# Performance work log

Measured on AMD Instinct MI355X. Metric: run time of the kernel, lower is better.

## Reference

```python
import jax, jax.numpy as jnp
import numpy as np

N, D = 8192, 128
ALPHA = 2.0


def setup_inputs() -> dict:
    key = jax.random.key(0)
    k1, k2, k3, k4 = jax.random.split(key, 4)
    z_au = jax.random.normal(k1, (N, D), dtype=jnp.float32)
    z_tp = jax.random.normal(k2, (N, D), dtype=jnp.float32)
    fc_weights = jax.random.normal(k3, (2, D), dtype=jnp.float32)
    labels = jax.random.randint(k4, (N,), 0, 2, dtype=jnp.int64)
    return {"z_au": z_au, "z_tp": z_tp, "fc_weights": fc_weights, "labels": labels}


def reference(z_au, z_tp, fc_weights, labels):
    # labels is unused in the (intended) math; kept for signature fidelity.
    n = z_au.shape[0]
    neg_inf = jnp.finfo(z_au.dtype).min
    eye = jnp.eye(n, dtype=bool)

    # pairwise dot-product similarities (cosim == raw matmul in the source)
    s_aa = z_au @ z_au.T              # [n, n]
    s_tt = z_tp @ z_tp.T              # [n, n]
    s_at = z_au @ z_tp.T              # [n, n]

    # pos_loss(i) = log( sum_{j!=i} exp(au_i.au_j) + exp(tp_i.tp_j) )
    pos_logits = jnp.concatenate(
        [jnp.where(eye, neg_inf, s_aa), jnp.where(eye, neg_inf, s_tt)], axis=1
    )                                  # [n, 2n]
    pos = jax.nn.logsumexp(pos_logits, axis=1)          # [n]

    # neg_loss(i) = log( sum_{j!=i} exp(au_i.tp_j) )
    neg = jax.nn.logsumexp(jnp.where(eye, neg_inf, s_at), axis=1)  # [n]

    # alpha * cosim(au_i, tp_i)
    au_tp_diag = jnp.einsum("nd,nd->n", z_au, z_tp)      # [n]

    supcon = jnp.sum(-pos + neg + ALPHA * au_tp_diag)

    # prototype loss: reward same-class prototype, punish other-class prototype
    pt0, pt1 = fc_weights[0], fc_weights[1]
    pt_loss = jnp.sum(-z_au @ pt0 + z_au @ pt1 - z_tp @ pt1 + z_tp @ pt0) / n

    return (pt_loss + supcon) / (n + 2)
```

## Files before the change

kernel.cpp:

```cpp
#include <hip/hip_runtime.h>


typedef float f32x4 __attribute__((ext_vector_type(4)));
typedef __bf16 bf16x8 __attribute__((ext_vector_type(8)));

static constexpr int   N_ROWS = 8192;
static constexpr int   DIM    = 128;
static constexpr float SQRT_LOG2E = 1.2011224087864498f;
static constexpr float C2  = 32.0f;
static constexpr float LN2 = 0.6931471805599453f;


__device__ inline unsigned short f2bf_rne(float x) {
    unsigned u = __builtin_bit_cast(unsigned, x);
    u += 0x7fffu + ((u >> 16) & 1u);
    return (unsigned short)(u >> 16);
}

#define GLD16(gptr, lptr)                                                  \
    __builtin_amdgcn_global_load_lds(                                      \
        (const __attribute__((address_space(1))) void*)(gptr),             \
        (__attribute__((address_space(3))) void*)(lptr), 16, 0, 0)

__global__ void prep_kernel(const float* __restrict__ zau,
                            const float* __restrict__ ztp,
                            unsigned short* __restrict__ bau,
                            unsigned short* __restrict__ btp,
                            float* __restrict__ P, float* __restrict__ Ng,
                            float* __restrict__ acc, unsigned* __restrict__ done) {
    int gid  = blockIdx.x * blockDim.x + threadIdx.x;
    int base = gid * 4;
    float4 a = *reinterpret_cast<const float4*>(zau + base);
    float4 t = *reinterpret_cast<const float4*>(ztp + base);
    ushort4 ua, ut;
    ua.x = f2bf_rne(a.x * SQRT_LOG2E); ua.y = f2bf_rne(a.y * SQRT_LOG2E);
    ua.z = f2bf_rne(a.z * SQRT_LOG2E); ua.w = f2bf_rne(a.w * SQRT_LOG2E);
    ut.x = f2bf_rne(t.x * SQRT_LOG2E); ut.y = f2bf_rne(t.y * SQRT_LOG2E);
    ut.z = f2bf_rne(t.z * SQRT_LOG2E); ut.w = f2bf_rne(t.w * SQRT_LOG2E);
    *reinterpret_cast<ushort4*>(bau + base) = ua;
    *reinterpret_cast<ushort4*>(btp + base) = ut;
    if (gid < N_ROWS) { P[gid] = 0.0f; Ng[gid] = 0.0f; }
    if (gid == 0)     { acc[0] = 0.0f; acc[1] = 0.0f; done[0] = 0u; }
}

template<bool DIAG>
__device__ inline void accum2(const f32x4 (&a)[2][2], float (&dst)[2][4],
                              int r0w, int colp, int quad, int l15) {
#pragma unroll
    for (int mt = 0; mt < 2; mt++)
#pragma unroll
        for (int nt = 0; nt < 2; nt++)
#pragma unroll
            for (int r = 0; r < 4; r++) {
                float e = __builtin_amdgcn_exp2f(a[mt][nt][r]);
                if (DIAG) {
                    int grow = r0w + mt * 16 + quad * 4 + r;
                    int gcol = colp + nt * 16 + l15;
                    if (grow == gcol) e = 0.0f;
                }
                dst[mt][r] += e;
            }
}

__global__ __launch_bounds__(256, 3)
void score_kernel(const unsigned short* __restrict__ bau,
                  const unsigned short* __restrict__ btp,
                  float* __restrict__ P, float* __restrict__ Ng) {
    __shared__ __align__(16) unsigned short ldsA[16 * 512];
    __shared__ __align__(16) unsigned short ldsT[16 * 512];

    const int tid  = threadIdx.x;
    const int lane = tid & 63;
    const int wave = tid >> 6;
    const int quad = lane >> 4;
    const int l15  = lane & 15;
    const int rb   = blockIdx.x & 63;
    const int cs   = blockIdx.x >> 6;
    const int r0w  = rb * 128 + wave * 32;

    const int laneoff = l15 * 256 + quad * 16;


    bf16x8 aAu[2][4], aTp[2][4];
#pragma unroll
    for (int mt = 0; mt < 2; mt++) {
        int row = r0w + mt * 16 + l15;
        const unsigned short* pa = bau + row * DIM + quad * 8;
        const unsigned short* pt = btp + row * DIM + quad * 8;
#pragma unroll
        for (int k = 0; k < 4; k++) {
            aAu[mt][k] = *reinterpret_cast<const bf16x8*>(pa + k * 32);
            aTp[mt][k] = *reinterpret_cast<const bf16x8*>(pt + k * 32);
        }
    }

    float sP[2][4] = {{0.f,0.f,0.f,0.f},{0.f,0.f,0.f,0.f}};
    float sN[2][4] = {{0.f,0.f,0.f,0.f},{0.f,0.f,0.f,0.f}};

    for (int ct = 0; ct < 8; ct++) {
        const int colbase = cs * 512 + ct * 64;
        __syncthreads();
#pragma unroll
        for (int j = 0; j < 8; j++) {
            const int f   = wave * 8 + j;
            const int arr = f >> 4;
            const int nt  = (f >> 2) & 3;
            const int k   = f & 3;
            const char* gb = (const char*)(arr ? btp : bau)
                           + ((size_t)(colbase + nt * 16) << 8) + (k << 6);
            unsigned short* lb = (arr ? ldsT : ldsA) + ((nt * 4 + k) << 9);
            GLD16(gb + laneoff, lb);
        }
        __syncthreads();

        const bool diag = (colbase < r0w + 32) && (colbase + 64 > r0w);

#pragma unroll
        for (int np = 0; np < 2; np++) {
            f32x4 acc[2][2];
#pragma unroll
            for (int mt = 0; mt < 2; mt++)
#pragma unroll
                for (int nt = 0; nt < 2; nt++)
                    acc[mt][nt] = f32x4{-C2, -C2, -C2, -C2};
#pragma unroll
            for (int k = 0; k < 4; k++) {
                bf16x8 b0 = *reinterpret_cast<const bf16x8*>(
                    ldsA + (((np * 2 + 0) * 4 + k) << 9) + lane * 8);
                bf16x8 b1 = *reinterpret_cast<const bf16x8*>(
                    ldsA + (((np * 2 + 1) * 4 + k) << 9) + lane * 8);
#pragma unroll
                for (int mt = 0; mt < 2; mt++) {
                    acc[mt][0] = __builtin_amdgcn_mfma_f32_16x16x32_bf16(
                        aAu[mt][k], b0, acc[mt][0], 0, 0, 0);
                    acc[mt][1] = __builtin_amdgcn_mfma_f32_16x16x32_bf16(
                        aAu[mt][k], b1, acc[mt][1], 0, 0, 0);
                }
            }
            if (diag) accum2<true >(acc, sP, r0w, colbase + np * 32, quad, l15);
            else      accum2<false>(acc, sP, r0w, colbase + np * 32, quad, l15);
        }

#pragma unroll
        for (int np = 0; np < 2; np++) {
            f32x4 aT[2][2], aX[2][2];
#pragma unroll
            for (int mt = 0; mt < 2; mt++)
#pragma unroll
                for (int nt = 0; nt < 2; nt++) {
                    aT[mt][nt] = f32x4{-C2, -C2, -C2, -C2};
                    aX[mt][nt] = f32x4{-C2, -C2, -C2, -C2};
                }
#pragma unroll
            for (int k = 0; k < 4; k++) {
                bf16x8 b0 = *reinterpret_cast<const bf16x8*>(
                    ldsT + (((np * 2 + 0) * 4 + k) << 9) + lane * 8);
                bf16x8 b1 = *reinterpret_cast<const bf16x8*>(
                    ldsT + (((np * 2 + 1) * 4 + k) << 9) + lane * 8);
#pragma unroll
                for (int mt = 0; mt < 2; mt++) {
                    aT[mt][0] = __builtin_amdgcn_mfma_f32_16x16x32_bf16(
                        aTp[mt][k], b0, aT[mt][0], 0, 0, 0);
                    aX[mt][0] = __builtin_amdgcn_mfma_f32_16x16x32_bf16(
                        aAu[mt][k], b0, aX[mt][0], 0, 0, 0);
                    aT[mt][1] = __builtin_amdgcn_mfma_f32_16x16x32_bf16(
                        aTp[mt][k], b1, aT[mt][1], 0, 0, 0);
                    aX[mt][1] = __builtin_amdgcn_mfma_f32_16x16x32_bf16(
                        aAu[mt][k], b1, aX[mt][1], 0, 0, 0);
                }
            }
            if (diag) { accum2<true >(aT, sP, r0w, colbase + np * 32, quad, l15);
                        accum2<true >(aX, sN, r0w, colbase + np * 32, quad, l15); }
            else      { accum2<false>(aT, sP, r0w, colbase + np * 32, quad, l15);
                        accum2<false>(aX, sN, r0w, colbase + np * 32, quad, l15); }
        }
    }

#pragma unroll
    for (int mt = 0; mt < 2; mt++)
#pragma unroll
        for (int r = 0; r < 4; r++) {
            float p = sP[mt][r], ng = sN[mt][r];
            for (int m = 1; m < 16; m <<= 1) {
                p  += __shfl_xor(p,  m, 64);
                ng += __shfl_xor(ng, m, 64);
            }
            if (l15 == 0) {
                int row = r0w + mt * 16 + quad * 4 + r;
                atomicAdd(&P[row],  p);
                atomicAdd(&Ng[row], ng);
            }
        }
}

__global__ void finalize_kernel(const float* __restrict__ zau,
                                const float* __restrict__ ztp,
                                const float* __restrict__ fc,
                                const float* __restrict__ P,
                                const float* __restrict__ Ng,
                                float* __restrict__ acc,
                                unsigned* __restrict__ done,
                                float* __restrict__ out) {
    int tid     = threadIdx.x;
    int lane    = tid & 63;
    int wave_id = blockIdx.x * 4 + (tid >> 6);

    float2 w0 = *reinterpret_cast<const float2*>(fc + 2 * lane);
    float2 w1 = *reinterpret_cast<const float2*>(fc + 256 + 2 * lane);
    float wx = w1.x - w0.x, wy = w1.y - w0.y;

    float ptp = 0.0f, ssum = 0.0f;
    for (int j = 0; j < 8; j++) {
        int i = wave_id * 8 + j;
        float2 a = *reinterpret_cast<const float2*>(zau + i * DIM + 2 * lane);
        float2 t = *reinterpret_cast<const float2*>(ztp + i * DIM + 2 * lane);
        float d = a.x * t.x + a.y * t.y;
        ptp += (a.x - t.x) * wx + (a.y - t.y) * wy;
        for (int m = 1; m < 64; m <<= 1) d += __shfl_xor(d, m, 64);
        if (lane == 0) {
            float c = LN2 * (__builtin_amdgcn_logf(Ng[i]) -
                             __builtin_amdgcn_logf(P[i])) + 2.0f * d;
            ssum += c;
        }
    }
    for (int m = 1; m < 64; m <<= 1) ptp += __shfl_xor(ptp, m, 64);
    if (lane == 0) {
        atomicAdd(&acc[0], ssum);
        atomicAdd(&acc[1], ptp);
    }

    __syncthreads();
    if (tid == 0) {
        __threadfence();
        unsigned ticket = atomicAdd(done, 1u);
        if (ticket == gridDim.x - 1) {
            float a0 = atomicAdd(&acc[0], 0.0f);
            float a1 = atomicAdd(&acc[1], 0.0f);
            out[0] = (a1 / (float)N_ROWS + a0) / (float)(N_ROWS + 2);
        }
    }
}

extern "C" void kernel_launch(void* const* d_in, const int* in_sizes, int n_in,
                              void* d_out, int out_size, void* d_ws, size_t ws_size,
                              hipStream_t stream) {
    const float* zau = (const float*)d_in[0];
    const float* ztp = (const float*)d_in[1];
    const float* fc  = (const float*)d_in[2];
    float* out = (float*)d_out;

    char* ws = (char*)d_ws;
    unsigned short* bau = (unsigned short*)(ws);
    unsigned short* btp = (unsigned short*)(ws + 2097152);
    float*    P    = (float*)(ws + 4194304);
    float*    Ng   = (float*)(ws + 4227072);
    float*    acc  = (float*)(ws + 4259840);
    unsigned* done = (unsigned*)(ws + 4259848);

    prep_kernel<<<dim3(1024), dim3(256), 0, stream>>>(zau, ztp, bau, btp, P, Ng, acc, done);
    score_kernel<<<dim3(1024), dim3(256), 0, stream>>>(bau, btp, P, Ng);
    finalize_kernel<<<dim3(256), dim3(256), 0, stream>>>(zau, ztp, fc, P, Ng, acc, done, out);
}
```

Measured before the change: 158.4 us.

## Software-pipeline exp accumulation of previous tile behind next tile's loads

Halves the column tile from 64 to 32 and merges the two LDS buffers into one. Each tile's three score blocks (AA, TT, AT) are now kept in registers and exponentiated on the next iteration, while the next tile's global-to-LDS loads are in flight. The aim is to hide load latency and barrier stalls behind the exp2 work and to free LDS for higher occupancy. The cost is twice as many barrier rounds and more live accumulator registers. The first iteration also exponentiates the initial -C2 placeholder blocks, which adds a small spurious term to each row's sums.

```diff
diff --git a/kernel.cpp b/kernel.cpp
--- a/kernel.cpp
+++ b/kernel.cpp
@@ -44,7 +44,7 @@
 }
 
 template<bool DIAG>
-__device__ inline void accum2(const f32x4 (&a)[2][2], float (&dst)[2][4],
+__device__ inline void expacc(const f32x4 (&a)[2][2], float (&dst)[2][4],
                               int r0w, int colp, int quad, int l15) {
 #pragma unroll
     for (int mt = 0; mt < 2; mt++)
@@ -66,8 +66,7 @@
 void score_kernel(const unsigned short* __restrict__ bau,
                   const unsigned short* __restrict__ btp,
                   float* __restrict__ P, float* __restrict__ Ng) {
-    __shared__ __align__(16) unsigned short ldsA[16 * 512];
-    __shared__ __align__(16) unsigned short ldsT[16 * 512];
+    __shared__ __align__(16) unsigned short lds[16 * 512];
 
     const int tid  = threadIdx.x;
     const int lane = tid & 63;
@@ -80,7 +79,6 @@
 
     const int laneoff = l15 * 256 + quad * 16;
 
-
     bf16x8 aAu[2][4], aTp[2][4];
 #pragma unroll
     for (int mt = 0; mt < 2; mt++) {
@@ -97,82 +95,96 @@
     float sP[2][4] = {{0.f,0.f,0.f,0.f},{0.f,0.f,0.f,0.f}};
     float sN[2][4] = {{0.f,0.f,0.f,0.f},{0.f,0.f,0.f,0.f}};
 
-    for (int ct = 0; ct < 8; ct++) {
-        const int colbase = cs * 512 + ct * 64;
+    f32x4 pAA[2][2], pTT[2][2], pAT[2][2];
+#pragma unroll
+    for (int mt = 0; mt < 2; mt++)
+#pragma unroll
+        for (int nt = 0; nt < 2; nt++) {
+            pAA[mt][nt] = f32x4{-C2, -C2, -C2, -C2};
+            pTT[mt][nt] = f32x4{-C2, -C2, -C2, -C2};
+            pAT[mt][nt] = f32x4{-C2, -C2, -C2, -C2};
+        }
+    int prevcol = -100000;
+
+    for (int ct = 0; ct < 16; ct++) {
+        const int colbase = cs * 512 + ct * 32;
+
         __syncthreads();
 #pragma unroll
-        for (int j = 0; j < 8; j++) {
-            const int f   = wave * 8 + j;
-            const int arr = f >> 4;
-            const int nt  = (f >> 2) & 3;
+        for (int j = 0; j < 4; j++) {
+            const int f   = wave * 4 + j;
+            const int arr = f >> 3;
+            const int nt  = (f >> 2) & 1;
             const int k   = f & 3;
             const char* gb = (const char*)(arr ? btp : bau)
                            + ((size_t)(colbase + nt * 16) << 8) + (k << 6);
-            unsigned short* lb = (arr ? ldsT : ldsA) + ((nt * 4 + k) << 9);
-            GLD16(gb + laneoff, lb);
-        }
+            GLD16(gb + laneoff, lds + (f << 9));
+        }
+
+        {
+            const bool pd = (prevcol < r0w + 32) && (prevcol + 32 > r0w);
+            if (pd) {
+                expacc<true >(pAA, sP, r0w, prevcol, quad, l15);
+                expacc<true >(pTT, sP, r0w, prevcol, quad, l15);
+                expacc<true >(pAT, sN, r0w, prevcol, quad, l15);
+            } else {
+                expacc<false>(pAA, sP, r0w, prevcol, quad, l15);
+                expacc<false>(pTT, sP, r0w, prevcol, quad, l15);
+                expacc<false>(pAT, sN, r0w, prevcol, quad, l15);
+            }
+        }
+#pragma unroll
+        for (int mt = 0; mt < 2; mt++)
+#pragma unroll
+            for (int nt = 0; nt < 2; nt++) {
+                pAA[mt][nt] = f32x4{-C2, -C2, -C2, -C2};
+                pTT[mt][nt] = f32x4{-C2, -C2, -C2, -C2};
+                pAT[mt][nt] = f32x4{-C2, -C2, -C2, -C2};
+            }
+
         __syncthreads();
 
-        const bool diag = (colbase < r0w + 32) && (colbase + 64 > r0w);
-
-#pragma unroll
-        for (int np = 0; np < 2; np++) {
-            f32x4 acc[2][2];
-#pragma unroll
-            for (int mt = 0; mt < 2; mt++)
-#pragma unroll
-                for (int nt = 0; nt < 2; nt++)
-                    acc[mt][nt] = f32x4{-C2, -C2, -C2, -C2};
-#pragma unroll
-            for (int k = 0; k < 4; k++) {
-                bf16x8 b0 = *reinterpret_cast<const bf16x8*>(
-                    ldsA + (((np * 2 + 0) * 4 + k) << 9) + lane * 8);
-                bf16x8 b1 = *reinterpret_cast<const bf16x8*>(
-                    ldsA + (((np * 2 + 1) * 4 + k) << 9) + lane * 8);
-#pragma unroll
-                for (int mt = 0; mt < 2; mt++) {
-                    acc[mt][0] = __builtin_amdgcn_mfma_f32_16x16x32_bf16(
-                        aAu[mt][k], b0, acc[mt][0], 0, 0, 0);
-                    acc[mt][1] = __builtin_amdgcn_mfma_f32_16x16x32_bf16(
-                        aAu[mt][k], b1, acc[mt][1], 0, 0, 0);
-                }
-            }
-            if (diag) accum2<true >(acc, sP, r0w, colbase + np * 32, quad, l15);
-            else      accum2<false>(acc, sP, r0w, colbase + np * 32, quad, l15);
-        }
-
-#pragma unroll
-        for (int np = 0; np < 2; np++) {
-            f32x4 aT[2][2], aX[2][2];
-#pragma unroll
-            for (int mt = 0; mt < 2; mt++)
-#pragma unroll
-                for (int nt = 0; nt < 2; nt++) {
-                    aT[mt][nt] = f32x4{-C2, -C2, -C2, -C2};
-                    aX[mt][nt] = f32x4{-C2, -C2, -C2, -C2};
-                }
-#pragma unroll
-            for (int k = 0; k < 4; k++) {
-                bf16x8 b0 = *reinterpret_cast<const bf16x8*>(
-                    ldsT + (((np * 2 + 0) * 4 + k) << 9) + lane * 8);
-                bf16x8 b1 = *reinterpret_cast<const bf16x8*>(
-                    ldsT + (((np * 2 + 1) * 4 + k) << 9) + lane * 8);
-#pragma unroll
-                for (int mt = 0; mt < 2; mt++) {
-                    aT[mt][0] = __builtin_amdgcn_mfma_f32_16x16x32_bf16(
-                        aTp[mt][k], b0, aT[mt][0], 0, 0, 0);
-                    aX[mt][0] = __builtin_amdgcn_mfma_f32_16x16x32_bf16(
-                        aAu[mt][k], b0, aX[mt][0], 0, 0, 0);
-                    aT[mt][1] = __builtin_amdgcn_mfma_f32_16x16x32_bf16(
-                        aTp[mt][k], b1, aT[mt][1], 0, 0, 0);
-                    aX[mt][1] = __builtin_amdgcn_mfma_f32_16x16x32_bf16(
-                        aAu[mt][k], b1, aX[mt][1], 0, 0, 0);
-                }
-            }
-            if (diag) { accum2<true >(aT, sP, r0w, colbase + np * 32, quad, l15);
-                        accum2<true >(aX, sN, r0w, colbase + np * 32, quad, l15); }
-            else      { accum2<false>(aT, sP, r0w, colbase + np * 32, quad, l15);
-                        accum2<false>(aX, sN, r0w, colbase + np * 32, quad, l15); }
+#pragma unroll
+        for (int k = 0; k < 4; k++) {
+            bf16x8 b0 = *reinterpret_cast<const bf16x8*>(lds + ((0 + k) << 9) + lane * 8);
+            bf16x8 b1 = *reinterpret_cast<const bf16x8*>(lds + ((4 + k) << 9) + lane * 8);
+#pragma unroll
+            for (int mt = 0; mt < 2; mt++) {
+                pAA[mt][0] = __builtin_amdgcn_mfma_f32_16x16x32_bf16(
+                    aAu[mt][k], b0, pAA[mt][0], 0, 0, 0);
+                pAA[mt][1] = __builtin_amdgcn_mfma_f32_16x16x32_bf16(
+                    aAu[mt][k], b1, pAA[mt][1], 0, 0, 0);
+            }
+        }
+#pragma unroll
+        for (int k = 0; k < 4; k++) {
+            bf16x8 t0 = *reinterpret_cast<const bf16x8*>(lds + ((8  + k) << 9) + lane * 8);
+            bf16x8 t1 = *reinterpret_cast<const bf16x8*>(lds + ((12 + k) << 9) + lane * 8);
+#pragma unroll
+            for (int mt = 0; mt < 2; mt++) {
+                pTT[mt][0] = __builtin_amdgcn_mfma_f32_16x16x32_bf16(
+                    aTp[mt][k], t0, pTT[mt][0], 0, 0, 0);
+                pAT[mt][0] = __builtin_amdgcn_mfma_f32_16x16x32_bf16(
+                    aAu[mt][k], t0, pAT[mt][0], 0, 0, 0);
+                pTT[mt][1] = __builtin_amdgcn_mfma_f32_16x16x32_bf16(
+                    aTp[mt][k], t1, pTT[mt][1], 0, 0, 0);
+                pAT[mt][1] = __builtin_amdgcn_mfma_f32_16x16x32_bf16(
+                    aAu[mt][k], t1, pAT[mt][1], 0, 0, 0);
+            }
+        }
+        prevcol = colbase;
+    }
+
+    {
+        const bool pd = (prevcol < r0w + 32) && (prevcol + 32 > r0w);
+        if (pd) {
+            expacc<true >(pAA, sP, r0w, prevcol, quad, l15);
+            expacc<true >(pTT, sP, r0w, prevcol, quad, l15);
+            expacc<true >(pAT, sN, r0w, prevcol, quad, l15);
+        } else {
+            expacc<false>(pAA, sP, r0w, prevcol, quad, l15);
+            expacc<false>(pTT, sP, r0w, prevcol, quad, l15);
+            expacc<false>(pAT, sN, r0w, prevcol, quad, l15);
         }
     }
 
```

New measurement: 155.5 us. About the same (-1.8%).

## Load B operand fragments directly from global memory instead of staging via LDS

Applied to the files above, without the earlier changes.

Removes the shared-memory staging (global_load_lds plus two __syncthreads per tile) and has each wave load its B-operand bf16 fragments straight from global memory into registers, 32 columns at a time. The T-panel loads are issued before the exponentials of the previous product, so memory latency can overlap with the exp work. This drops block-wide barriers and the LDS footprint, which may raise occupancy. The cost is that each of the four waves now fetches the same column data separately, relying on L1/L2 hits, with more register pressure from the held fragments.

```diff
diff --git a/kernel.cpp b/kernel.cpp
--- a/kernel.cpp
+++ b/kernel.cpp
@@ -16,11 +16,6 @@
     u += 0x7fffu + ((u >> 16) & 1u);
     return (unsigned short)(u >> 16);
 }
-
-#define GLD16(gptr, lptr)                                                  \
-    __builtin_amdgcn_global_load_lds(                                      \
-        (const __attribute__((address_space(1))) void*)(gptr),             \
-        (__attribute__((address_space(3))) void*)(lptr), 16, 0, 0)
 
 __global__ void prep_kernel(const float* __restrict__ zau,
                             const float* __restrict__ ztp,
@@ -44,7 +39,7 @@
 }
 
 template<bool DIAG>
-__device__ inline void accum2(const f32x4 (&a)[2][2], float (&dst)[2][4],
+__device__ inline void expacc(const f32x4 (&a)[2][2], float (&dst)[2][4],
                               int r0w, int colp, int quad, int l15) {
 #pragma unroll
     for (int mt = 0; mt < 2; mt++)
@@ -66,9 +61,6 @@
 void score_kernel(const unsigned short* __restrict__ bau,
                   const unsigned short* __restrict__ btp,
                   float* __restrict__ P, float* __restrict__ Ng) {
-    __shared__ __align__(16) unsigned short ldsA[16 * 512];
-    __shared__ __align__(16) unsigned short ldsT[16 * 512];
-
     const int tid  = threadIdx.x;
     const int lane = tid & 63;
     const int wave = tid >> 6;
@@ -78,9 +70,6 @@
     const int cs   = blockIdx.x >> 6;
     const int r0w  = rb * 128 + wave * 32;
 
-    const int laneoff = l15 * 256 + quad * 16;
-
-
     bf16x8 aAu[2][4], aTp[2][4];
 #pragma unroll
     for (int mt = 0; mt < 2; mt++) {
@@ -97,83 +86,77 @@
     float sP[2][4] = {{0.f,0.f,0.f,0.f},{0.f,0.f,0.f,0.f}};
     float sN[2][4] = {{0.f,0.f,0.f,0.f},{0.f,0.f,0.f,0.f}};
 
-    for (int ct = 0; ct < 8; ct++) {
-        const int colbase = cs * 512 + ct * 64;
-        __syncthreads();
-#pragma unroll
-        for (int j = 0; j < 8; j++) {
-            const int f   = wave * 8 + j;
-            const int arr = f >> 4;
-            const int nt  = (f >> 2) & 3;
-            const int k   = f & 3;
-            const char* gb = (const char*)(arr ? btp : bau)
-                           + ((size_t)(colbase + nt * 16) << 8) + (k << 6);
-            unsigned short* lb = (arr ? ldsT : ldsA) + ((nt * 4 + k) << 9);
-            GLD16(gb + laneoff, lb);
-        }
-        __syncthreads();
-
-        const bool diag = (colbase < r0w + 32) && (colbase + 64 > r0w);
-
-#pragma unroll
-        for (int np = 0; np < 2; np++) {
-            f32x4 acc[2][2];
-#pragma unroll
-            for (int mt = 0; mt < 2; mt++)
-#pragma unroll
-                for (int nt = 0; nt < 2; nt++)
-                    acc[mt][nt] = f32x4{-C2, -C2, -C2, -C2};
-#pragma unroll
-            for (int k = 0; k < 4; k++) {
-                bf16x8 b0 = *reinterpret_cast<const bf16x8*>(
-                    ldsA + (((np * 2 + 0) * 4 + k) << 9) + lane * 8);
-                bf16x8 b1 = *reinterpret_cast<const bf16x8*>(
-                    ldsA + (((np * 2 + 1) * 4 + k) << 9) + lane * 8);
-#pragma unroll
-                for (int mt = 0; mt < 2; mt++) {
-                    acc[mt][0] = __builtin_amdgcn_mfma_f32_16x16x32_bf16(
-                        aAu[mt][k], b0, acc[mt][0], 0, 0, 0);
-                    acc[mt][1] = __builtin_amdgcn_mfma_f32_16x16x32_bf16(
-                        aAu[mt][k], b1, acc[mt][1], 0, 0, 0);
-                }
-            }
-            if (diag) accum2<true >(acc, sP, r0w, colbase + np * 32, quad, l15);
-            else      accum2<false>(acc, sP, r0w, colbase + np * 32, quad, l15);
-        }
-
-#pragma unroll
-        for (int np = 0; np < 2; np++) {
-            f32x4 aT[2][2], aX[2][2];
-#pragma unroll
-            for (int mt = 0; mt < 2; mt++)
-#pragma unroll
-                for (int nt = 0; nt < 2; nt++) {
-                    aT[mt][nt] = f32x4{-C2, -C2, -C2, -C2};
-                    aX[mt][nt] = f32x4{-C2, -C2, -C2, -C2};
-                }
-#pragma unroll
-            for (int k = 0; k < 4; k++) {
-                bf16x8 b0 = *reinterpret_cast<const bf16x8*>(
-                    ldsT + (((np * 2 + 0) * 4 + k) << 9) + lane * 8);
-                bf16x8 b1 = *reinterpret_cast<const bf16x8*>(
-                    ldsT + (((np * 2 + 1) * 4 + k) << 9) + lane * 8);
-#pragma unroll
-                for (int mt = 0; mt < 2; mt++) {
-                    aT[mt][0] = __builtin_amdgcn_mfma_f32_16x16x32_bf16(
-                        aTp[mt][k], b0, aT[mt][0], 0, 0, 0);
-                    aX[mt][0] = __builtin_amdgcn_mfma_f32_16x16x32_bf16(
-                        aAu[mt][k], b0, aX[mt][0], 0, 0, 0);
-                    aT[mt][1] = __builtin_amdgcn_mfma_f32_16x16x32_bf16(
-                        aTp[mt][k], b1, aT[mt][1], 0, 0, 0);
-                    aX[mt][1] = __builtin_amdgcn_mfma_f32_16x16x32_bf16(
-                        aAu[mt][k], b1, aX[mt][1], 0, 0, 0);
-                }
-            }
-            if (diag) { accum2<true >(aT, sP, r0w, colbase + np * 32, quad, l15);
-                        accum2<true >(aX, sN, r0w, colbase + np * 32, quad, l15); }
-            else      { accum2<false>(aT, sP, r0w, colbase + np * 32, quad, l15);
-                        accum2<false>(aX, sN, r0w, colbase + np * 32, quad, l15); }
-        }
+    const int laneElem = l15 * DIM + quad * 8;
+    const unsigned short* panAu = bau + (size_t)cs * 512 * DIM + laneElem;
+    const unsigned short* panTp = btp + (size_t)cs * 512 * DIM + laneElem;
+
+    for (int ct = 0; ct < 16; ct++) {
+        const int colbase = cs * 512 + ct * 32;
+        const unsigned short* pa = panAu + ct * 32 * DIM;
+        const unsigned short* pt = panTp + ct * 32 * DIM;
+        const bool diag = (colbase < r0w + 32) && (colbase + 32 > r0w);
+
+        bf16x8 bA[2][4];
+#pragma unroll
+        for (int nt = 0; nt < 2; nt++)
+#pragma unroll
+            for (int k = 0; k < 4; k++)
+                bA[nt][k] = *reinterpret_cast<const bf16x8*>(
+                    pa + nt * 16 * DIM + k * 32);
+
+        f32x4 accA[2][2];
+#pragma unroll
+        for (int mt = 0; mt < 2; mt++)
+#pragma unroll
+            for (int nt = 0; nt < 2; nt++)
+                accA[mt][nt] = f32x4{-C2, -C2, -C2, -C2};
+#pragma unroll
+        for (int k = 0; k < 4; k++)
+#pragma unroll
+            for (int mt = 0; mt < 2; mt++) {
+                accA[mt][0] = __builtin_amdgcn_mfma_f32_16x16x32_bf16(
+                    aAu[mt][k], bA[0][k], accA[mt][0], 0, 0, 0);
+                accA[mt][1] = __builtin_amdgcn_mfma_f32_16x16x32_bf16(
+                    aAu[mt][k], bA[1][k], accA[mt][1], 0, 0, 0);
+            }
+
+        bf16x8 bT[2][4];
+#pragma unroll
+        for (int nt = 0; nt < 2; nt++)
+#pragma unroll
+            for (int k = 0; k < 4; k++)
+                bT[nt][k] = *reinterpret_cast<const bf16x8*>(
+                    pt + nt * 16 * DIM + k * 32);
+
+        if (diag) expacc<true >(accA, sP, r0w, colbase, quad, l15);
+        else      expacc<false>(accA, sP, r0w, colbase, quad, l15);
+
+        f32x4 accT[2][2], accX[2][2];
+#pragma unroll
+        for (int mt = 0; mt < 2; mt++)
+#pragma unroll
+            for (int nt = 0; nt < 2; nt++) {
+                accT[mt][nt] = f32x4{-C2, -C2, -C2, -C2};
+                accX[mt][nt] = f32x4{-C2, -C2, -C2, -C2};
+            }
+#pragma unroll
+        for (int k = 0; k < 4; k++)
+#pragma unroll
+            for (int mt = 0; mt < 2; mt++) {
+                accT[mt][0] = __builtin_amdgcn_mfma_f32_16x16x32_bf16(
+                    aTp[mt][k], bT[0][k], accT[mt][0], 0, 0, 0);
+                accX[mt][0] = __builtin_amdgcn_mfma_f32_16x16x32_bf16(
+                    aAu[mt][k], bT[0][k], accX[mt][0], 0, 0, 0);
+                accT[mt][1] = __builtin_amdgcn_mfma_f32_16x16x32_bf16(
+                    aTp[mt][k], bT[1][k], accT[mt][1], 0, 0, 0);
+                accX[mt][1] = __builtin_amdgcn_mfma_f32_16x16x32_bf16(
+                    aAu[mt][k], bT[1][k], accX[mt][1], 0, 0, 0);
+            }
+
+        if (diag) { expacc<true >(accT, sP, r0w, colbase, quad, l15);
+                    expacc<true >(accX, sN, r0w, colbase, quad, l15); }
+        else      { expacc<false>(accT, sP, r0w, colbase, quad, l15);
+                    expacc<false>(accX, sN, r0w, colbase, quad, l15); }
     }
 
 #pragma unroll
```

New measurement: 222.6 us. 1.4x slower.
